# Performance work log

Measured on AMD Instinct MI355X. Metric: run time of the kernel, lower is better.

## Reference

```python
import jax, jax.numpy as jnp
import numpy as np

INPUT_SIZE = 40960
HIDDEN_SIZE = 128
OUTPUT_SIZE = 1
BATCH = 4096


def setup_inputs() -> dict:
    key = jax.random.key(0)
    k1, k2, k3, kw1, kw2, kw3 = jax.random.split(key, 6)
    x1 = jax.random.uniform(k1, (BATCH, INPUT_SIZE), dtype=jnp.float32)
    x2 = jax.random.uniform(k2, (BATCH, INPUT_SIZE), dtype=jnp.float32)
    turn = jax.random.randint(k3, (BATCH,), 0, 2, dtype=jnp.int32)
    # nn.Linear weights: [out_features, in_features], kaiming-uniform-ish scale
    s1 = 1.0 / np.sqrt(INPUT_SIZE)
    s2 = 1.0 / np.sqrt(2 * HIDDEN_SIZE)
    w_us = jax.random.uniform(kw1, (HIDDEN_SIZE, INPUT_SIZE), minval=-s1, maxval=s1, dtype=jnp.float32)
    w_them = jax.random.uniform(kw2, (HIDDEN_SIZE, INPUT_SIZE), minval=-s1, maxval=s1, dtype=jnp.float32)
    w2 = jax.random.uniform(kw3, (OUTPUT_SIZE, 2 * HIDDEN_SIZE), minval=-s2, maxval=s2, dtype=jnp.float32)
    return {"x1": x1, "x2": x2, "turn": turn, "w_us": w_us, "w_them": w_them, "w2": w2}


def reference(x1, x2, turn, w_us, w_them, w2):
    # acc1 = relu(fc1_us(x1)); acc2 = relu(fc1_them(x2))
    acc1 = jax.nn.relu(jnp.einsum('bi,hi->bh', x1, w_us))   # [B, H]
    acc2 = jax.nn.relu(jnp.einsum('bi,hi->bh', x2, w_them)) # [B, H]
    x = jnp.concatenate((acc1, acc2), axis=1)               # [B, 2H]
    return jnp.einsum('bh,oh->bo', x, w2)                   # [B, 1]
```

## Files before the change

kernel.cpp:

```cpp
#include <hip/hip_runtime.h>

#define B_ROWS 4096
#define K_DIM  40960
#define H_DIM  128
#define BM     128
#define BK     64
#define KSPLIT 8
#define KCHUNK (K_DIM / KSPLIT)
#define NT     (KCHUNK / BK)
#define MT     (B_ROWS / BM)

typedef __attribute__((ext_vector_type(4))) float f32x4;
typedef __attribute__((ext_vector_type(8))) short short8;

static_assert(KSPLIT * KCHUNK == K_DIM, "ksplit");
static_assert((NT & 1) == 0, "NT even");

__device__ float g_acc[2u * B_ROWS * H_DIM];

__device__ __forceinline__ unsigned pkbf(float a, float b) {
  unsigned ua = __float_as_uint(a), ub = __float_as_uint(b);
  ua = (ua + 0x7fffu + ((ua >> 16) & 1u)) >> 16;
  ub = (ub + 0x7fffu + ((ub >> 16) & 1u)) & 0xffff0000u;
  return ua | ub;
}

template <bool ATOMIC>
__global__ __launch_bounds__(512, 4) void nnue_stage1(
    const float* __restrict__ x1, const float* __restrict__ x2,
    const float* __restrict__ wus, const float* __restrict__ wthem,
    float* __restrict__ part) {
  __shared__ ushort ldsA[2][BM][BK];
  __shared__ ushort ldsB[2][H_DIM][BK];

  const int t = threadIdx.x;

  const int bid  = blockIdx.x;
  const int xcd  = bid & 7;
  const int slot = bid >> 3;
  const int g    = xcd + 8 * (slot >> 5);
  const int mt   = slot & 31;
  const int mat  = g & 1;
  const int ks   = g >> 1;

  const float* __restrict__ X = mat ? x2 : x1;
  const float* __restrict__ W = mat ? wthem : wus;

  const int lrow = t >> 4;
  const int kf   = (t & 15) * 4;
  const size_t kbase = (size_t)ks * KCHUNK + kf;
  const float* gA = X + ((size_t)mt * BM + lrow) * K_DIM + kbase;
  const float* gB = W + (size_t)lrow * K_DIM + kbase;

  int wb[4];
  {
    const int slot0 = (t & 15) >> 1;
    const int rem   = (t & 1) * 8;
    #pragma unroll
    for (int r = 0; r < 4; ++r) {
      const int row = lrow + 32 * r;
      wb[r] = row * (BK * 2) + ((slot0 ^ (row & 7)) * 16) + rem;
    }
  }

  const int lane = t & 63;
  const int wid  = t >> 6;
  const int wr   = wid >> 2;
  const int wc   = wid & 3;
  const int fr   = lane & 15;
  const int lhi  = lane >> 4;

  int offA[4], offB[2];
  #pragma unroll
  for (int i = 0; i < 4; ++i) {
    const int row = wr * 64 + i * 16 + fr;
    offA[i] = row * (BK * 2) + ((lhi ^ (row & 7)) * 16);
  }
  #pragma unroll
  for (int j = 0; j < 2; ++j) {
    const int row = wc * 32 + j * 16 + fr;
    offB[j] = row * (BK * 2) + ((lhi ^ (row & 7)) * 16);
  }

  f32x4 acc[4][2] = {};
  f32x4 ra[4], rb[4];

#define LOADT(kt_)                                                          \
  do {                                                                      \
    const float* pa = gA + (size_t)(kt_)*BK;                                \
    const float* pb = gB + (size_t)(kt_)*BK;                                \
    _Pragma("unroll") for (int r = 0; r < 4; ++r) {                         \
      ra[r] = __builtin_nontemporal_load(                                   \
          (const f32x4*)(pa + (size_t)r * 32 * K_DIM));                     \
      rb[r] = *(const f32x4*)(pb + (size_t)r * 32 * K_DIM);                 \
    }                                                                       \
  } while (0)

#define STAGE(buf_)                                                         \
  do {                                                                      \
    char* baseA = (char*)(&ldsA[buf_][0][0]);                               \
    char* baseB = (char*)(&ldsB[buf_][0][0]);                               \
    _Pragma("unroll") for (int r = 0; r < 4; ++r) {                         \
      uint2 pA, pB;                                                         \
      pA.x = pkbf(ra[r].x, ra[r].y);                                        \
      pA.y = pkbf(ra[r].z, ra[r].w);                                        \
      pB.x = pkbf(rb[r].x, rb[r].y);                                        \
      pB.y = pkbf(rb[r].z, rb[r].w);                                        \
      *(uint2*)(baseA + wb[r]) = pA;                                        \
      *(uint2*)(baseB + wb[r]) = pB;                                        \
    }                                                                       \
  } while (0)

#define MFMA_STEP(buf_)                                                     \
  do {                                                                      \
    const char* baseA = (const char*)(&ldsA[buf_][0][0]);                   \
    const char* baseB = (const char*)(&ldsB[buf_][0][0]);                   \
    _Pragma("unroll") for (int kb = 0; kb < 2; ++kb) {                      \
      short8 af[4], bg[2];                                                  \
      _Pragma("unroll") for (int i = 0; i < 4; ++i)                         \
          af[i] = *(const short8*)(baseA + (offA[i] ^ (kb * 64)));          \
      _Pragma("unroll") for (int j = 0; j < 2; ++j)                         \
          bg[j] = *(const short8*)(baseB + (offB[j] ^ (kb * 64)));          \
      _Pragma("unroll") for (int i = 0; i < 4; ++i)                         \
          _Pragma("unroll") for (int j = 0; j < 2; ++j)                     \
              acc[i][j] = __builtin_amdgcn_mfma_f32_16x16x32_bf16(          \
                  af[i], bg[j], acc[i][j], 0, 0, 0);                        \
    }                                                                       \
  } while (0)

  LOADT(0);
  STAGE(0);
  __syncthreads();

  for (int kt = 0; kt < NT; kt += 2) {
    LOADT(kt + 1);
    MFMA_STEP(0);
    STAGE(1);
    __syncthreads();
    if (kt + 2 < NT) {
      LOADT(kt + 2);
      MFMA_STEP(1);
      STAGE(0);
      __syncthreads();
    } else {
      MFMA_STEP(1);
    }
  }

  const int browg = mt * BM + wr * 64;
  if (!ATOMIC) {
    float* dst = part + (((size_t)mat * KSPLIT + ks) * B_ROWS) * (size_t)H_DIM;
    #pragma unroll
    for (int i = 0; i < 4; ++i)
      #pragma unroll
      for (int j = 0; j < 2; ++j)
        #pragma unroll
        for (int r = 0; r < 4; ++r) {
          const int rowg = browg + i * 16 + (lhi << 2) + r;
          const int colg = wc * 32 + j * 16 + fr;
          __builtin_nontemporal_store(acc[i][j][r],
                                      &dst[(size_t)rowg * H_DIM + colg]);
        }
  } else {
    float* dst = g_acc + (size_t)mat * B_ROWS * H_DIM;
    #pragma unroll
    for (int i = 0; i < 4; ++i)
      #pragma unroll
      for (int j = 0; j < 2; ++j)
        #pragma unroll
        for (int r = 0; r < 4; ++r) {
          const int rowg = browg + i * 16 + (lhi << 2) + r;
          const int colg = wc * 32 + j * 16 + fr;
          atomicAdd(&dst[(size_t)rowg * H_DIM + colg], acc[i][j][r]);
        }
  }
#undef LOADT
#undef STAGE
#undef MFMA_STEP
}

__global__ void nnue_zero_acc() {
  const unsigned i = blockIdx.x * 256 + threadIdx.x;
  if (i < 2u * B_ROWS * H_DIM) g_acc[i] = 0.f;
}

template <int KS>
__global__ __launch_bounds__(512) void nnue_stage2(
    const float* __restrict__ part, const float* __restrict__ w2,
    float* __restrict__ out) {
  const float* p = part ? part : (const float*)g_acc;
  const int t = threadIdx.x;
  const int l = t & 63, w = t >> 6;
  const int b = blockIdx.x * 8 + w;
  float a0 = 0.f, a1 = 0.f, a2 = 0.f, a3 = 0.f;
  #pragma unroll
  for (int ks = 0; ks < KS; ++ks) {
    const float* p0 = p + ((size_t)ks * B_ROWS + b) * H_DIM;
    const float* p1 = p + (((size_t)KS + ks) * B_ROWS + b) * H_DIM;
    a0 += __builtin_nontemporal_load(&p0[l]);
    a1 += __builtin_nontemporal_load(&p0[l + 64]);
    a2 += __builtin_nontemporal_load(&p1[l]);
    a3 += __builtin_nontemporal_load(&p1[l + 64]);
  }
  float s = fmaxf(a0, 0.f) * w2[l] + fmaxf(a1, 0.f) * w2[l + 64] +
            fmaxf(a2, 0.f) * w2[l + 128] + fmaxf(a3, 0.f) * w2[l + 192];
  #pragma unroll
  for (int off = 32; off; off >>= 1) s += __shfl_xor(s, off, 64);
  if (l == 0) out[b] = s;
}

extern "C" void kernel_launch(void* const* d_in, const int* in_sizes, int n_in,
                              void* d_out, int out_size, void* d_ws,
                              size_t ws_size, hipStream_t stream) {
  const float* x1    = (const float*)d_in[0];
  const float* x2    = (const float*)d_in[1];
  const float* wus   = (const float*)d_in[3];
  const float* wthem = (const float*)d_in[4];
  const float* w2    = (const float*)d_in[5];
  float* out = (float*)d_out;

  const size_t PART_BYTES =
      2ull * KSPLIT * B_ROWS * H_DIM * sizeof(float);

  if (ws_size >= PART_BYTES) {
    float* part = (float*)d_ws;
    nnue_stage1<false><<<MT * KSPLIT * 2, 512, 0, stream>>>(x1, x2, wus, wthem,
                                                            part);
    nnue_stage2<KSPLIT><<<B_ROWS / 8, 512, 0, stream>>>(part, w2, out);
  } else {
    nnue_zero_acc<<<(2 * B_ROWS * H_DIM + 255) / 256, 256, 0, stream>>>();
    nnue_stage1<true><<<MT * KSPLIT * 2, 512, 0, stream>>>(x1, x2, wus, wthem,
                                                           nullptr);
    nnue_stage2<1><<<B_ROWS / 8, 512, 0, stream>>>(nullptr, w2, out);
  }
}
```

Baseline: 300.9 us.

## Load activation tile directly to registers, stage only weights through LDS

```diff
diff --git a/kernel.cpp b/kernel.cpp
--- a/kernel.cpp
+++ b/kernel.cpp
@@ -3,7 +3,7 @@
 #define B_ROWS 4096
 #define K_DIM  40960
 #define H_DIM  128
-#define BM     128
+#define BM     64
 #define BK     64
 #define KSPLIT 8
 #define KCHUNK (K_DIM / KSPLIT)
@@ -25,158 +25,166 @@
   return ua | ub;
 }
 
+__device__ __forceinline__ short8 pk8(f32x4 a, f32x4 b) {
+  union { unsigned u[4]; short8 s; } r;
+  r.u[0] = pkbf(a[0], a[1]);
+  r.u[1] = pkbf(a[2], a[3]);
+  r.u[2] = pkbf(b[0], b[1]);
+  r.u[3] = pkbf(b[2], b[3]);
+  return r.s;
+}
+
 template <bool ATOMIC>
-__global__ __launch_bounds__(512, 4) void nnue_stage1(
+__global__ __launch_bounds__(256, 4) void nnue_stage1(
     const float* __restrict__ x1, const float* __restrict__ x2,
     const float* __restrict__ wus, const float* __restrict__ wthem,
     float* __restrict__ part) {
-  __shared__ ushort ldsA[2][BM][BK];
   __shared__ ushort ldsB[2][H_DIM][BK];
 
   const int t = threadIdx.x;
 
-  const int bid  = blockIdx.x;
-  const int xcd  = bid & 7;
-  const int slot = bid >> 3;
-  const int g    = xcd + 8 * (slot >> 5);
-  const int mt   = slot & 31;
-  const int mat  = g & 1;
-  const int ks   = g >> 1;
+  const int bid = blockIdx.x;
+  const int xcd = bid & 7;
+  const int s   = bid >> 3;
+  const int mt  = s & 63;
+  const int g   = xcd | ((s >> 6) << 3);
+  const int mat = g & 1;
+  const int ks  = g >> 1;
 
   const float* __restrict__ X = mat ? x2 : x1;
   const float* __restrict__ W = mat ? wthem : wus;
-
-  const int lrow = t >> 4;
-  const int kf   = (t & 15) * 4;
-  const size_t kbase = (size_t)ks * KCHUNK + kf;
-  const float* gA = X + ((size_t)mt * BM + lrow) * K_DIM + kbase;
-  const float* gB = W + (size_t)lrow * K_DIM + kbase;
-
-  int wb[4];
-  {
-    const int slot0 = (t & 15) >> 1;
-    const int rem   = (t & 1) * 8;
-    #pragma unroll
-    for (int r = 0; r < 4; ++r) {
-      const int row = lrow + 32 * r;
-      wb[r] = row * (BK * 2) + ((slot0 ^ (row & 7)) * 16) + rem;
-    }
-  }
+  const size_t kbase = (size_t)ks * KCHUNK;
 
   const int lane = t & 63;
-  const int wid  = t >> 6;
-  const int wr   = wid >> 2;
-  const int wc   = wid & 3;
+  const int w    = t >> 6;
   const int fr   = lane & 15;
   const int lhi  = lane >> 4;
 
-  int offA[4], offB[2];
+  const int arow = mt * BM + w * 16 + fr;
+  const float* gA = X + (size_t)arow * K_DIM + kbase + lhi * 8;
+
+  const int r0   = t >> 4;
+  const int slot = t & 15;
+  const float* gBq[4];
   #pragma unroll
-  for (int i = 0; i < 4; ++i) {
-    const int row = wr * 64 + i * 16 + fr;
-    offA[i] = row * (BK * 2) + ((lhi ^ (row & 7)) * 16);
-  }
-  #pragma unroll
-  for (int j = 0; j < 2; ++j) {
-    const int row = wc * 32 + j * 16 + fr;
-    offB[j] = row * (BK * 2) + ((lhi ^ (row & 7)) * 16);
-  }
-
-  f32x4 acc[4][2] = {};
-  f32x4 ra[4], rb[4];
-
-#define LOADT(kt_)                                                          \
+  for (int q = 0; q < 4; ++q)
+    gBq[q] = W + (size_t)(r0 + 16 * q) * K_DIM + kbase + slot * 4;
+  const int wb0 = r0 * 128 + ((((slot >> 1) ^ (r0 & 7)) << 4)) + ((slot & 1) << 3);
+
+  const int offb0 = fr * 128 + ((lhi ^ (fr & 7)) << 4);
+  const int offb1 = offb0 ^ 64;
+
+  char* ldsbase = (char*)(&ldsB[0][0][0]);
+
+  f32x4 acc[8] = {};
+  f32x4 rawA[4], rawB[4];
+  f32x4 btmp[4];
+
+#define LOADA(raw_, kt_)                                                    \
   do {                                                                      \
     const float* pa = gA + (size_t)(kt_)*BK;                                \
-    const float* pb = gB + (size_t)(kt_)*BK;                                \
-    _Pragma("unroll") for (int r = 0; r < 4; ++r) {                         \
-      ra[r] = __builtin_nontemporal_load(                                   \
-          (const f32x4*)(pa + (size_t)r * 32 * K_DIM));                     \
-      rb[r] = *(const f32x4*)(pb + (size_t)r * 32 * K_DIM);                 \
-    }                                                                       \
-  } while (0)
-
-#define STAGE(buf_)                                                         \
-  do {                                                                      \
-    char* baseA = (char*)(&ldsA[buf_][0][0]);                               \
-    char* baseB = (char*)(&ldsB[buf_][0][0]);                               \
-    _Pragma("unroll") for (int r = 0; r < 4; ++r) {                         \
-      uint2 pA, pB;                                                         \
-      pA.x = pkbf(ra[r].x, ra[r].y);                                        \
-      pA.y = pkbf(ra[r].z, ra[r].w);                                        \
-      pB.x = pkbf(rb[r].x, rb[r].y);                                        \
-      pB.y = pkbf(rb[r].z, rb[r].w);                                        \
-      *(uint2*)(baseA + wb[r]) = pA;                                        \
-      *(uint2*)(baseB + wb[r]) = pB;                                        \
-    }                                                                       \
-  } while (0)
-
-#define MFMA_STEP(buf_)                                                     \
-  do {                                                                      \
-    const char* baseA = (const char*)(&ldsA[buf_][0][0]);                   \
-    const char* baseB = (const char*)(&ldsB[buf_][0][0]);                   \
-    _Pragma("unroll") for (int kb = 0; kb < 2; ++kb) {                      \
-      short8 af[4], bg[2];                                                  \
-      _Pragma("unroll") for (int i = 0; i < 4; ++i)                         \
-          af[i] = *(const short8*)(baseA + (offA[i] ^ (kb * 64)));          \
-      _Pragma("unroll") for (int j = 0; j < 2; ++j)                         \
-          bg[j] = *(const short8*)(baseB + (offB[j] ^ (kb * 64)));          \
-      _Pragma("unroll") for (int i = 0; i < 4; ++i)                         \
-          _Pragma("unroll") for (int j = 0; j < 2; ++j)                     \
-              acc[i][j] = __builtin_amdgcn_mfma_f32_16x16x32_bf16(          \
-                  af[i], bg[j], acc[i][j], 0, 0, 0);                        \
-    }                                                                       \
-  } while (0)
-
-  LOADT(0);
-  STAGE(0);
-  __syncthreads();
-
-  for (int kt = 0; kt < NT; kt += 2) {
-    LOADT(kt + 1);
-    MFMA_STEP(0);
-    STAGE(1);
-    __syncthreads();
-    if (kt + 2 < NT) {
-      LOADT(kt + 2);
-      MFMA_STEP(1);
-      STAGE(0);
-      __syncthreads();
-    } else {
-      MFMA_STEP(1);
-    }
-  }
-
-  const int browg = mt * BM + wr * 64;
+    raw_[0] = __builtin_nontemporal_load((const f32x4*)(pa));               \
+    raw_[1] = __builtin_nontemporal_load((const f32x4*)(pa + 4));           \
+    raw_[2] = __builtin_nontemporal_load((const f32x4*)(pa + 32));          \
+    raw_[3] = __builtin_nontemporal_load((const f32x4*)(pa + 36));          \
+  } while (0)
+
+#define LOADB_H(h_, kt_)                                                    \
+  do {                                                                      \
+    _Pragma("unroll") for (int q = 0; q < 4; ++q)                           \
+        btmp[q] = *(const f32x4*)(gBq[q] + (size_t)(h_)*64 * K_DIM +        \
+                                  (size_t)(kt_)*BK);                        \
+  } while (0)
+
+#define STAGEB_H(h_, buf_)                                                  \
+  do {                                                                      \
+    _Pragma("unroll") for (int q = 0; q < 4; ++q) {                         \
+      uint2 p;                                                              \
+      p.x = pkbf(btmp[q][0], btmp[q][1]);                                   \
+      p.y = pkbf(btmp[q][2], btmp[q][3]);                                   \
+      *(uint2*)(ldsbase + wb0 + q * 2048 + (h_)*8192 + (buf_)*16384) = p;   \
+    }                                                                       \
+  } while (0)
+
+#define MFMA_KB(buf_, af_, OFFB_)                                           \
+  do {                                                                      \
+    _Pragma("unroll") for (int j = 0; j < 8; ++j) {                         \
+      short8 bg =                                                           \
+          *(const short8*)(ldsbase + (OFFB_) + j * 2048 + (buf_)*16384);    \
+      acc[j] =                                                              \
+          __builtin_amdgcn_mfma_f32_16x16x32_bf16(af_, bg, acc[j], 0, 0, 0);\
+    }                                                                       \
+  } while (0)
+
+#define BARRIER()                                                           \
+  do {                                                                      \
+    asm volatile("s_waitcnt lgkmcnt(0)" ::: "memory");                      \
+    __builtin_amdgcn_s_barrier();                                           \
+    __builtin_amdgcn_sched_barrier(0);                                      \
+  } while (0)
+
+#define TILE(raw_, BUFC_, BUFN_, ktn_, kta_, DO_A, DO_B)                    \
+  do {                                                                      \
+    short8 af0 = pk8(raw_[0], raw_[1]);                                     \
+    short8 af1 = pk8(raw_[2], raw_[3]);                                     \
+    if (DO_A) LOADA(raw_, kta_);                                            \
+    if (DO_B) LOADB_H(0, ktn_);                                             \
+    MFMA_KB(BUFC_, af0, offb0);                                             \
+    if (DO_B) {                                                             \
+      STAGEB_H(0, BUFN_);                                                   \
+      LOADB_H(1, ktn_);                                                     \
+    }                                                                       \
+    MFMA_KB(BUFC_, af1, offb1);                                             \
+    if (DO_B) {                                                             \
+      STAGEB_H(1, BUFN_);                                                   \
+      BARRIER();                                                            \
+    }                                                                       \
+  } while (0)
+
+  LOADA(rawA, 0);
+  LOADA(rawB, 1);
+  LOADB_H(0, 0);
+  STAGEB_H(0, 0);
+  LOADB_H(1, 0);
+  STAGEB_H(1, 0);
+  BARRIER();
+
+  for (int kt = 0; kt < NT - 2; kt += 2) {
+    TILE(rawA, 0, 1, kt + 1, kt + 2, true, true);
+    TILE(rawB, 1, 0, kt + 2, kt + 3, true, true);
+  }
+  TILE(rawA, 0, 1, NT - 1, 0, false, true);
+  TILE(rawB, 1, 0, 0, 0, false, false);
+
+#undef LOADA
+#undef LOADB_H
+#undef STAGEB_H
+#undef MFMA_KB
+#undef BARRIER
+#undef TILE
+
   if (!ATOMIC) {
     float* dst = part + (((size_t)mat * KSPLIT + ks) * B_ROWS) * (size_t)H_DIM;
     #pragma unroll
-    for (int i = 0; i < 4; ++i)
+    for (int j = 0; j < 8; ++j)
       #pragma unroll
-      for (int j = 0; j < 2; ++j)
-        #pragma unroll
-        for (int r = 0; r < 4; ++r) {
-          const int rowg = browg + i * 16 + (lhi << 2) + r;
-          const int colg = wc * 32 + j * 16 + fr;
-          __builtin_nontemporal_store(acc[i][j][r],
-                                      &dst[(size_t)rowg * H_DIM + colg]);
-        }
+      for (int r = 0; r < 4; ++r) {
+        const int rowg = mt * BM + w * 16 + (lhi << 2) + r;
+        const int colg = j * 16 + fr;
+        __builtin_nontemporal_store(acc[j][r],
+                                    &dst[(size_t)rowg * H_DIM + colg]);
+      }
   } else {
     float* dst = g_acc + (size_t)mat * B_ROWS * H_DIM;
     #pragma unroll
-    for (int i = 0; i < 4; ++i)
+    for (int j = 0; j < 8; ++j)
       #pragma unroll
-      for (int j = 0; j < 2; ++j)
-        #pragma unroll
-        for (int r = 0; r < 4; ++r) {
-          const int rowg = browg + i * 16 + (lhi << 2) + r;
-          const int colg = wc * 32 + j * 16 + fr;
-          atomicAdd(&dst[(size_t)rowg * H_DIM + colg], acc[i][j][r]);
-        }
-  }
-#undef LOADT
-#undef STAGE
-#undef MFMA_STEP
+      for (int r = 0; r < 4; ++r) {
+        const int rowg = mt * BM + w * 16 + (lhi << 2) + r;
+        const int colg = j * 16 + fr;
+        atomicAdd(&dst[(size_t)rowg * H_DIM + colg], acc[j][r]);
+      }
+  }
 }
 
 __global__ void nnue_zero_acc() {
@@ -202,11 +210,11 @@
     a2 += __builtin_nontemporal_load(&p1[l]);
     a3 += __builtin_nontemporal_load(&p1[l + 64]);
   }
-  float s = fmaxf(a0, 0.f) * w2[l] + fmaxf(a1, 0.f) * w2[l + 64] +
-            fmaxf(a2, 0.f) * w2[l + 128] + fmaxf(a3, 0.f) * w2[l + 192];
+  float sv = fmaxf(a0, 0.f) * w2[l] + fmaxf(a1, 0.f) * w2[l + 64] +
+             fmaxf(a2, 0.f) * w2[l + 128] + fmaxf(a3, 0.f) * w2[l + 192];
   #pragma unroll
-  for (int off = 32; off; off >>= 1) s += __shfl_xor(s, off, 64);
-  if (l == 0) out[b] = s;
+  for (int off = 32; off; off >>= 1) sv += __shfl_xor(sv, off, 64);
+  if (l == 0) out[b] = sv;
 }
 
 extern "C" void kernel_launch(void* const* d_in, const int* in_sizes, int n_in,
@@ -224,12 +232,12 @@
 
   if (ws_size >= PART_BYTES) {
     float* part = (float*)d_ws;
-    nnue_stage1<false><<<MT * KSPLIT * 2, 512, 0, stream>>>(x1, x2, wus, wthem,
+    nnue_stage1<false><<<MT * KSPLIT * 2, 256, 0, stream>>>(x1, x2, wus, wthem,
                                                             part);
     nnue_stage2<KSPLIT><<<B_ROWS / 8, 512, 0, stream>>>(part, w2, out);
   } else {
     nnue_zero_acc<<<(2 * B_ROWS * H_DIM + 255) / 256, 256, 0, stream>>>();
-    nnue_stage1<true><<<MT * KSPLIT * 2, 512, 0, stream>>>(x1, x2, wus, wthem,
+    nnue_stage1<true><<<MT * KSPLIT * 2, 256, 0, stream>>>(x1, x2, wus, wthem,
                                                            nullptr);
     nnue_stage2<1><<<B_ROWS / 8, 512, 0, stream>>>(nullptr, w2, out);
   }
```

Result: slower. 412.7 us (+37.1%).

## Stream fp32 tiles directly to LDS via global_load_lds and convert at fragment read

Applied to the files above, without the earlier changes.

```diff
diff --git a/kernel.cpp b/kernel.cpp
--- a/kernel.cpp
+++ b/kernel.cpp
@@ -5,7 +5,7 @@
 #define H_DIM  128
 #define BM     128
 #define BK     64
-#define KSPLIT 8
+#define KSPLIT 4
 #define KCHUNK (K_DIM / KSPLIT)
 #define NT     (KCHUNK / BK)
 #define MT     (B_ROWS / BM)
@@ -25,102 +25,97 @@
   return ua | ub;
 }
 
+__device__ __forceinline__ short8 pk8f4(float4 a, float4 b) {
+  union { unsigned u[4]; short8 s; } r;
+  r.u[0] = pkbf(a.x, a.y);
+  r.u[1] = pkbf(a.z, a.w);
+  r.u[2] = pkbf(b.x, b.y);
+  r.u[3] = pkbf(b.z, b.w);
+  return r.s;
+}
+
 template <bool ATOMIC>
-__global__ __launch_bounds__(512, 4) void nnue_stage1(
+__global__ __launch_bounds__(512, 2) void nnue_stage1(
     const float* __restrict__ x1, const float* __restrict__ x2,
     const float* __restrict__ wus, const float* __restrict__ wthem,
     float* __restrict__ part) {
-  __shared__ ushort ldsA[2][BM][BK];
-  __shared__ ushort ldsB[2][H_DIM][BK];
+  __shared__ float ldsA[2][BM][BK];
+  __shared__ float ldsB[2][H_DIM][BK];
 
   const int t = threadIdx.x;
 
-  const int bid  = blockIdx.x;
-  const int xcd  = bid & 7;
-  const int slot = bid >> 3;
-  const int g    = xcd + 8 * (slot >> 5);
-  const int mt   = slot & 31;
-  const int mat  = g & 1;
-  const int ks   = g >> 1;
+  const int bid = blockIdx.x;
+  const int g   = bid & 7;
+  const int mt  = bid >> 3;
+  const int mat = g & 1;
+  const int ks  = g >> 1;
 
   const float* __restrict__ X = mat ? x2 : x1;
   const float* __restrict__ W = mat ? wthem : wus;
-
-  const int lrow = t >> 4;
-  const int kf   = (t & 15) * 4;
-  const size_t kbase = (size_t)ks * KCHUNK + kf;
-  const float* gA = X + ((size_t)mt * BM + lrow) * K_DIM + kbase;
-  const float* gB = W + (size_t)lrow * K_DIM + kbase;
-
-  int wb[4];
-  {
-    const int slot0 = (t & 15) >> 1;
-    const int rem   = (t & 1) * 8;
-    #pragma unroll
-    for (int r = 0; r < 4; ++r) {
-      const int row = lrow + 32 * r;
-      wb[r] = row * (BK * 2) + ((slot0 ^ (row & 7)) * 16) + rem;
-    }
-  }
-
-  const int lane = t & 63;
-  const int wid  = t >> 6;
-  const int wr   = wid >> 2;
-  const int wc   = wid & 3;
-  const int fr   = lane & 15;
-  const int lhi  = lane >> 4;
+  const size_t kb0 = (size_t)ks * KCHUNK;
+
+  const int l = t & 63;
+  const int w = t >> 6;
+
+  const float* gAq[4];
+  const float* gBq[4];
+  #pragma unroll
+  for (int q = 0; q < 4; ++q) {
+    const int r = (w * 4 + q) * 4 + (l >> 4);
+    const int c = (l & 15) ^ (r & 7);
+    gAq[q] = X + ((size_t)(mt * BM + r)) * K_DIM + kb0 + c * 4;
+    gBq[q] = W + (size_t)r * K_DIM + kb0 + c * 4;
+  }
+
+  const int wr  = w >> 2;
+  const int wc  = w & 3;
+  const int fr  = l & 15;
+  const int lhi = l >> 4;
 
   int offA[4], offB[2];
   #pragma unroll
   for (int i = 0; i < 4; ++i) {
-    const int row = wr * 64 + i * 16 + fr;
-    offA[i] = row * (BK * 2) + ((lhi ^ (row & 7)) * 16);
+    const int ra = wr * 64 + i * 16 + fr;
+    offA[i] = ra * 256 + (((lhi * 2) ^ (ra & 7)) << 4);
   }
   #pragma unroll
   for (int j = 0; j < 2; ++j) {
-    const int row = wc * 32 + j * 16 + fr;
-    offB[j] = row * (BK * 2) + ((lhi ^ (row & 7)) * 16);
+    const int cb = wc * 32 + j * 16 + fr;
+    offB[j] = cb * 256 + (((lhi * 2) ^ (cb & 7)) << 4);
   }
 
   f32x4 acc[4][2] = {};
-  f32x4 ra[4], rb[4];
-
-#define LOADT(kt_)                                                          \
+
+#define GLOAD(g_, l_)                                                       \
+  __builtin_amdgcn_global_load_lds(                                         \
+      (const __attribute__((address_space(1))) void*)(g_),                  \
+      (__attribute__((address_space(3))) void*)(l_), 16, 0, 0)
+
+#define ISSUE(buf_, kf_)                                                    \
   do {                                                                      \
-    const float* pa = gA + (size_t)(kt_)*BK;                                \
-    const float* pb = gB + (size_t)(kt_)*BK;                                \
-    _Pragma("unroll") for (int r = 0; r < 4; ++r) {                         \
-      ra[r] = __builtin_nontemporal_load(                                   \
-          (const f32x4*)(pa + (size_t)r * 32 * K_DIM));                     \
-      rb[r] = *(const f32x4*)(pb + (size_t)r * 32 * K_DIM);                 \
+    _Pragma("unroll") for (int q = 0; q < 4; ++q) {                         \
+      GLOAD(gAq[q] + (kf_), &ldsA[buf_][(w * 4 + q) * 4][0]);               \
+      GLOAD(gBq[q] + (kf_), &ldsB[buf_][(w * 4 + q) * 4][0]);               \
     }                                                                       \
   } while (0)
 
-#define STAGE(buf_)                                                         \
+#define COMPUTE(buf_)                                                       \
   do {                                                                      \
-    char* baseA = (char*)(&ldsA[buf_][0][0]);                               \
-    char* baseB = (char*)(&ldsB[buf_][0][0]);                               \
-    _Pragma("unroll") for (int r = 0; r < 4; ++r) {                         \
-      uint2 pA, pB;                                                         \
-      pA.x = pkbf(ra[r].x, ra[r].y);                                        \
-      pA.y = pkbf(ra[r].z, ra[r].w);                                        \
-      pB.x = pkbf(rb[r].x, rb[r].y);                                        \
-      pB.y = pkbf(rb[r].z, rb[r].w);                                        \
-      *(uint2*)(baseA + wb[r]) = pA;                                        \
-      *(uint2*)(baseB + wb[r]) = pB;                                        \
-    }                                                                       \
-  } while (0)
-
-#define MFMA_STEP(buf_)                                                     \
-  do {                                                                      \
-    const char* baseA = (const char*)(&ldsA[buf_][0][0]);                   \
-    const char* baseB = (const char*)(&ldsB[buf_][0][0]);                   \
+    const char* bA = (const char*)(&ldsA[buf_][0][0]);                      \
+    const char* bB = (const char*)(&ldsB[buf_][0][0]);                      \
     _Pragma("unroll") for (int kb = 0; kb < 2; ++kb) {                      \
+      const int kx = kb * 128;                                              \
       short8 af[4], bg[2];                                                  \
-      _Pragma("unroll") for (int i = 0; i < 4; ++i)                         \
-          af[i] = *(const short8*)(baseA + (offA[i] ^ (kb * 64)));          \
-      _Pragma("unroll") for (int j = 0; j < 2; ++j)                         \
-          bg[j] = *(const short8*)(baseB + (offB[j] ^ (kb * 64)));          \
+      _Pragma("unroll") for (int i = 0; i < 4; ++i) {                       \
+        float4 u = *(const float4*)(bA + (offA[i] ^ kx));                   \
+        float4 v = *(const float4*)(bA + (offA[i] ^ kx ^ 16));              \
+        af[i] = pk8f4(u, v);                                                \
+      }                                                                     \
+      _Pragma("unroll") for (int j = 0; j < 2; ++j) {                       \
+        float4 u = *(const float4*)(bB + (offB[j] ^ kx));                   \
+        float4 v = *(const float4*)(bB + (offB[j] ^ kx ^ 16));              \
+        bg[j] = pk8f4(u, v);                                                \
+      }                                                                     \
       _Pragma("unroll") for (int i = 0; i < 4; ++i)                         \
           _Pragma("unroll") for (int j = 0; j < 2; ++j)                     \
               acc[i][j] = __builtin_amdgcn_mfma_f32_16x16x32_bf16(          \
@@ -128,26 +123,36 @@
     }                                                                       \
   } while (0)
 
-  LOADT(0);
-  STAGE(0);
-  __syncthreads();
-
-  for (int kt = 0; kt < NT; kt += 2) {
-    LOADT(kt + 1);
-    MFMA_STEP(0);
-    STAGE(1);
-    __syncthreads();
-    if (kt + 2 < NT) {
-      LOADT(kt + 2);
-      MFMA_STEP(1);
-      STAGE(0);
-      __syncthreads();
-    } else {
-      MFMA_STEP(1);
-    }
-  }
-
-  const int browg = mt * BM + wr * 64;
+#define WAIT_BAR(n_)                                                        \
+  do {                                                                      \
+    asm volatile("s_waitcnt vmcnt(" #n_ ")" ::: "memory");                  \
+    __builtin_amdgcn_s_barrier();                                           \
+    __builtin_amdgcn_sched_barrier(0);                                      \
+  } while (0)
+
+  ISSUE(0, 0);
+  ISSUE(1, 64);
+
+  int kf = 0;
+  for (int kt = 0; kt < NT - 2; ++kt, kf += 64) {
+    const int buf = kt & 1;
+    WAIT_BAR(8);
+    COMPUTE(buf);
+    __builtin_amdgcn_sched_barrier(0);
+    __builtin_amdgcn_s_barrier();
+    ISSUE(buf, kf + 128);
+  }
+  WAIT_BAR(8);
+  COMPUTE((NT - 2) & 1);
+  __builtin_amdgcn_sched_barrier(0);
+  WAIT_BAR(0);
+  COMPUTE((NT - 1) & 1);
+
+#undef GLOAD
+#undef ISSUE
+#undef COMPUTE
+#undef WAIT_BAR
+
   if (!ATOMIC) {
     float* dst = part + (((size_t)mat * KSPLIT + ks) * B_ROWS) * (size_t)H_DIM;
     #pragma unroll
@@ -156,7 +161,7 @@
       for (int j = 0; j < 2; ++j)
         #pragma unroll
         for (int r = 0; r < 4; ++r) {
-          const int rowg = browg + i * 16 + (lhi << 2) + r;
+          const int rowg = mt * BM + wr * 64 + i * 16 + (lhi << 2) + r;
           const int colg = wc * 32 + j * 16 + fr;
           __builtin_nontemporal_store(acc[i][j][r],
                                       &dst[(size_t)rowg * H_DIM + colg]);
@@ -169,14 +174,11 @@
       for (int j = 0; j < 2; ++j)
         #pragma unroll
         for (int r = 0; r < 4; ++r) {
-          const int rowg = browg + i * 16 + (lhi << 2) + r;
+          const int rowg = mt * BM + wr * 64 + i * 16 + (lhi << 2) + r;
           const int colg = wc * 32 + j * 16 + fr;
           atomicAdd(&dst[(size_t)rowg * H_DIM + colg], acc[i][j][r]);
         }
   }
-#undef LOADT
-#undef STAGE
-#undef MFMA_STEP
 }
 
 __global__ void nnue_zero_acc() {
@@ -202,11 +204,11 @@
     a2 += __builtin_nontemporal_load(&p1[l]);
     a3 += __builtin_nontemporal_load(&p1[l + 64]);
   }
-  float s = fmaxf(a0, 0.f) * w2[l] + fmaxf(a1, 0.f) * w2[l + 64] +
-            fmaxf(a2, 0.f) * w2[l + 128] + fmaxf(a3, 0.f) * w2[l + 192];
-  #pragma unroll
-  for (int off = 32; off; off >>= 1) s += __shfl_xor(s, off, 64);
-  if (l == 0) out[b] = s;
+  float sv = fmaxf(a0, 0.f) * w2[l] + fmaxf(a1, 0.f) * w2[l + 64] +
+             fmaxf(a2, 0.f) * w2[l + 128] + fmaxf(a3, 0.f) * w2[l + 192];
+  #pragma unroll
+  for (int off = 32; off; off >>= 1) sv += __shfl_xor(sv, off, 64);
+  if (l == 0) out[b] = sv;
 }
 
 extern "C" void kernel_launch(void* const* d_in, const int* in_sizes, int n_in,
```

Measured after the change: 457.0 us. +51.9%, slower.
